# Kernel optimization log

Hardware: AMD Instinct MI355X
Metric: run time of the kernel (lower is better)

Reference implementation:

```python
import jax, jax.numpy as jnp
import numpy as np
import math

L, H, P = 16384, 128, 256


def setup_inputs() -> dict:
    key = jax.random.key(0)
    k = jax.random.split(key, 6)
    return {
        "input_sequence": jax.random.normal(k[0], (L, H), dtype=jnp.float32),
        "A_diag": jax.random.uniform(k[1], (P,), dtype=jnp.float32),
        "B": (jax.random.uniform(k[2], (P, H, 2), dtype=jnp.float32) * 2.0 - 1.0) / math.sqrt(H),
        "C": (jax.random.uniform(k[3], (H, P, 2), dtype=jnp.float32) * 2.0 - 1.0) / math.sqrt(P),
        "D": jax.random.normal(k[4], (H,), dtype=jnp.float32),
        "steps": jax.random.uniform(k[5], (P,), dtype=jnp.float32),
    }


def _binop(qi, qj):
    # 2x2 block-diagonal matrix product + affine state propagation, per channel.
    iA, iB, iC, iD, ib1, ib2 = qi
    jA, jB, jC, jD, jb1, jb2 = qj
    return (
        jA * iA + jB * iC,
        jA * iB + jB * iD,
        jC * iA + jD * iC,
        jC * iB + jD * iD,
        jA * ib1 + jB * ib2 + jb1,
        jC * ib1 + jD * ib2 + jb2,
    )


def reference(input_sequence, A_diag, B, C, D, steps):
    # LinOSS-IM discretization (implicit)
    A = jax.nn.relu(A_diag)                      # (P,)
    dt = jax.nn.sigmoid(steps)                   # (P,)
    Bc = B[..., 0] + 1j * B[..., 1]              # (P,H) complex64
    Cc = C[..., 0] + 1j * C[..., 1]              # (H,P) complex64

    Bu = input_sequence @ Bc.T                   # (L,P) complex64

    schur = 1.0 / (1.0 + dt ** 2 * A)
    M11 = 1.0 - dt ** 2 * A * schur
    M12 = -dt * A * schur
    M21 = dt * schur
    M22 = schur

    ones = jnp.ones((input_sequence.shape[0], A.shape[0]), dtype=input_sequence.dtype)
    F1 = M11 * Bu * dt                           # (L,P) complex
    F2 = M21 * Bu * dt

    elems = (M11 * ones, M12 * ones, M21 * ones, M22 * ones, F1, F2)
    _, _, _, _, _, x2 = jax.lax.associative_scan(_binop, elems)  # scan over L

    ys = jnp.real(x2 @ Cc.T)                     # (L,H)
    return ys + input_sequence * D
```

## Files before the change

kernel.cpp:

```cpp
#include <hip/hip_runtime.h>
#include <math.h>

#define L 16384
#define H 128
#define P 256
#define CL 32
#define NCH (L/CL)
#define GS 16
#define NG (NCH/GS)
#define KDIM 512
#define NBU 512

typedef __attribute__((ext_vector_type(8))) short short8;
typedef __attribute__((ext_vector_type(4))) float f32x4;

__device__ inline unsigned short f2bf(float f){
  union { float f; unsigned u; } v; v.f = f;
  unsigned u = v.u;
  u += 0x7fffu + ((u >> 16) & 1u);
  return (unsigned short)(u >> 16);
}
__device__ inline float bf2f(unsigned short s){
  union { unsigned u; float f; } v; v.u = ((unsigned)s) << 16;
  return v.f;
}

struct Params { float M11,M12,M21,M22,s1,s2; };

__device__ inline Params get_params(const float* A_diag, const float* steps, int p){
  float A = A_diag[p]; A = A > 0.f ? A : 0.f;
  float dt = 1.f/(1.f + expf(-steps[p]));
  float schur = 1.f/(1.f + dt*dt*A);
  Params q;
  q.M11 = 1.f - dt*dt*A*schur;
  q.M12 = -dt*A*schur;
  q.M21 = dt*schur;
  q.M22 = schur;
  q.s1 = q.M11*dt;
  q.s2 = q.M21*dt;
  return q;
}

__device__ inline unsigned long long aload(const unsigned long long* p){
  return __hip_atomic_load((unsigned long long*)p, __ATOMIC_RELAXED,
                           __HIP_MEMORY_SCOPE_AGENT);
}
__device__ inline void apub(unsigned long long* p, unsigned long long v){
  (void)__hip_atomic_exchange(p, v, __ATOMIC_RELAXED, __HIP_MEMORY_SCOPE_AGENT);
}
__device__ inline void fpub(unsigned* p){
  (void)__hip_atomic_exchange(p, 1u, __ATOMIC_RELAXED, __HIP_MEMORY_SCOPE_AGENT);
}
__device__ inline void wait_flag(unsigned* f){
  while (__hip_atomic_load(f, __ATOMIC_RELAXED, __HIP_MEMORY_SCOPE_AGENT) == 0u)
    __builtin_amdgcn_s_sleep(1);
}

__device__ inline void chunk_bu_to_lds(int c, const float* __restrict__ in,
                                       const unsigned short* __restrict__ BWswz,
                                       unsigned short (*sBu)[NBU+8]){
  int tid = threadIdx.x;
  int lane = tid & 63, w = tid >> 6;
  int ml = lane & 15, quad = lane >> 4;
  int mt = w & 1, ng = w >> 1;
  int lm0 = mt*16;
  const float* aptr = in + (size_t)(c*CL + lm0 + ml)*H + quad*8;
  short8 av[4];
  #pragma unroll
  for (int ks=0; ks<4; ks++){
    float4 f0 = *(const float4*)(aptr + ks*32);
    float4 f1 = *(const float4*)(aptr + ks*32 + 4);
    union { short8 s; unsigned short u[8]; } o;
    o.u[0]=f2bf(f0.x); o.u[1]=f2bf(f0.y); o.u[2]=f2bf(f0.z); o.u[3]=f2bf(f0.w);
    o.u[4]=f2bf(f1.x); o.u[5]=f2bf(f1.y); o.u[6]=f2bf(f1.z); o.u[7]=f2bf(f1.w);
    av[ks] = o.s;
  }
  f32x4 acc[8];
  #pragma unroll
  for (int t=0;t<8;t++) acc[t] = (f32x4){0.f,0.f,0.f,0.f};
  #pragma unroll
  for (int ks=0; ks<4; ks++){
    #pragma unroll
    for (int t=0;t<8;t++){
      int n0 = (ng*8 + t)*16;
      short8 bv = *(const short8*)(BWswz + ((size_t)(ks*4+quad)*NBU + n0 + ml)*8);
      acc[t] = __builtin_amdgcn_mfma_f32_16x16x32_bf16(av[ks], bv, acc[t], 0, 0, 0);
    }
  }
  #pragma unroll
  for (int t=0;t<8;t++){
    int n = (ng*8+t)*16 + ml;
    #pragma unroll
    for (int r=0;r<4;r++)
      sBu[lm0 + quad*4 + r][n] = f2bf(acc[t][r]);
  }
}

__global__ __launch_bounds__(512) void prep_w(const float* __restrict__ B,
                                              const float* __restrict__ Cw,
                                              unsigned short* __restrict__ BWswz,
                                              unsigned short* __restrict__ Bswz,
                                              unsigned* __restrict__ flags){
  int gidx = blockIdx.x*512 + threadIdx.x;
  if (gidx < NCH + NG + 1) flags[gidx] = 0u;
  if (gidx < H*NBU){
    int k = gidx >> 9, n = gidx & 511;
    int p = n & 255, c2 = n >> 8;
    float v = B[((size_t)p*H + k)*2 + c2];
    BWswz[((size_t)(k>>3)*NBU + n)*8 + (k&7)] = f2bf(v);
  } else {
    int g2 = gidx - H*NBU;
    int k = g2 >> 7, n = g2 & 127;
    float v = (k < P) ? Cw[((size_t)n*P + k)*2]
                      : -Cw[((size_t)n*P + (k-P))*2 + 1];
    Bswz[((size_t)(k>>3)*H + n)*8 + (k&7)] = f2bf(v);
  }
}

__global__ __launch_bounds__(512, 4) void linoss_fused(
    const float* __restrict__ in,
    const float* __restrict__ A_diag,
    const float* __restrict__ steps,
    const float* __restrict__ Dv,
    const unsigned short* __restrict__ BWswz,
    const unsigned short* __restrict__ Bswz,
    unsigned long long* __restrict__ finals,
    unsigned long long* __restrict__ gfin,
    unsigned* __restrict__ flag1,
    unsigned* __restrict__ flag2,
    unsigned* __restrict__ counter,
    float* __restrict__ out)
{
  __shared__ unsigned short sX[CL][NBU+8];
  __shared__ int s_cid;
  const int tid = threadIdx.x;
  if (tid == 0)
    s_cid = (int)__hip_atomic_fetch_add(counter, 1u, __ATOMIC_RELAXED,
                                        __HIP_MEMORY_SCOPE_AGENT);
  __syncthreads();
  const int c = s_cid;

  chunk_bu_to_lds(c, in, BWswz, sX);
  __syncthreads();

  const int p = tid & 255, part = tid >> 8;
  Params q = get_params(A_diag, steps, p);
  float Ta=q.M11, Tb=q.M12, Tc=q.M21, Td=q.M22;
  #pragma unroll
  for (int s=0;s<5;s++){
    float na=Ta*Ta+Tb*Tc, nb=Ta*Tb+Tb*Td, nc=Tc*Ta+Td*Tc, nd=Tc*Tb+Td*Td;
    Ta=na;Tb=nb;Tc=nc;Td=nd;
  }
  float fx1=0.f, fx2=0.f;
  {
    float u[CL];
    #pragma unroll
    for (int i=0;i<CL;i++) u[i] = bf2f(sX[i][part*256 + p]);
    #pragma unroll
    for (int i=0;i<CL;i++){
      float n1 = q.M11*fx1 + q.M12*fx2 + q.s1*u[i];
      float n2 = q.M21*fx1 + q.M22*fx2 + q.s2*u[i];
      fx1 = n1; fx2 = n2;
    }
  }
  {
    union { unsigned long long u; float2 f; } w; w.f = make_float2(fx1,fx2);
    apub(&finals[(size_t)(part*NCH + c)*P + p], w.u);
  }
  asm volatile("s_waitcnt vmcnt(0)" ::: "memory");
  __syncthreads();
  if (tid == 0) fpub(&flag1[c]);

  const int g = c >> 4, iw = c & (GS-1);
  const unsigned long long* Fp = finals + (size_t)part*NCH*P + (size_t)g*GS*P + p;

  float z1=0.f, z2v=0.f;
  bool have_z = false;
  if (iw == GS-1){
    if (tid < GS-1) wait_flag(&flag1[g*GS + tid]);
    __syncthreads();
    unsigned long long v[GS-1];
    #pragma unroll
    for (int j=0;j<GS-1;j++) v[j] = aload(Fp + (size_t)j*P);
    #pragma unroll
    for (int j=0;j<GS-1;j++){
      union { unsigned long long u; float2 f; } w; w.u = v[j];
      float n1 = Ta*z1 + Tb*z2v + w.f.x;
      float n2 = Tc*z1 + Td*z2v + w.f.y;
      z1=n1; z2v=n2;
    }
    have_z = true;
    float t1 = Ta*z1 + Tb*z2v + fx1;
    float t2 = Tc*z1 + Td*z2v + fx2;
    union { unsigned long long u; float2 f; } w; w.f = make_float2(t1,t2);
    apub(&gfin[(size_t)(part*NG + g)*P + p], w.u);
    asm volatile("s_waitcnt vmcnt(0)" ::: "memory");
    __syncthreads();
    if (tid == 0) fpub(&flag2[g]);
  }

  float sa=1.f, sb=0.f, sc=0.f, sd=1.f;
  {
    float wa=Ta, wb=Tb, wc=Tc, wd=Td;
    #pragma unroll
    for (int bit=0; bit<4; bit++){
      if ((iw>>bit)&1){
        float na = wa*sa + wb*sc, nb = wa*sb + wb*sd;
        float nc = wc*sa + wd*sc, nd = wc*sb + wd*sd;
        sa=na; sb=nb; sc=nc; sd=nd;
      }
      float qa = wa*wa + wb*wc, qb = wa*wb + wb*wd;
      float qc = wc*wa + wd*wc, qd = wc*wb + wd*wd;
      wa=qa; wb=qb; wc=qc; wd=qd;
    }
  }
  float ga=Ta, gb=Tb, gc=Tc, gd=Td;
  #pragma unroll
  for (int s=0;s<4;s++){
    float na=ga*ga+gb*gc, nb=ga*gb+gb*gd, nc=gc*ga+gd*gc, nd=gc*gb+gd*gd;
    ga=na;gb=nb;gc=nc;gd=nd;
  }

  if (tid < g)                             wait_flag(&flag2[tid]);
  if (!have_z && tid >= 64 && tid < 64+iw) wait_flag(&flag1[g*GS + (tid-64)]);
  __syncthreads();

  {
    float y1=0.f, y2=0.f;
    {
      const unsigned long long* Gp = gfin + (size_t)part*NG*P + p;
      #pragma unroll
      for (int half=0; half<2; half++){
        unsigned long long v[16];
        #pragma unroll
        for (int j=0;j<16;j++) v[j] = aload(Gp + (size_t)(half*16+j)*P);
        #pragma unroll
        for (int j=0;j<16;j++){
          int jj = half*16+j;
          if (jj < g){
            union { unsigned long long u; float2 f; } w; w.u = v[j];
            float n1 = ga*y1 + gb*y2 + w.f.x;
            float n2 = gc*y1 + gd*y2 + w.f.y;
            y1=n1; y2=n2;
          }
        }
      }
    }
    if (!have_z){
      unsigned long long v[GS-1];
      #pragma unroll
      for (int j=0;j<GS-1;j++) v[j] = aload(Fp + (size_t)j*P);
      #pragma unroll
      for (int j=0;j<GS-1;j++){
        if (j < iw){
          union { unsigned long long u; float2 f; } w; w.u = v[j];
          float n1 = Ta*z1 + Tb*z2v + w.f.x;
          float n2 = Tc*z1 + Td*z2v + w.f.y;
          z1=n1; z2v=n2;
        }
      }
    }
    float x1 = sa*y1 + sb*y2 + z1;
    float x2 = sc*y1 + sd*y2 + z2v;
    float u[CL];
    #pragma unroll
    for (int i=0;i<CL;i++) u[i] = bf2f(sX[i][part*256 + p]);
    unsigned short hw[CL];
    #pragma unroll
    for (int i=0;i<CL;i++){
      float n1 = q.M11*x1 + q.M12*x2 + q.s1*u[i];
      float n2 = q.M21*x1 + q.M22*x2 + q.s2*u[i];
      x1 = n1; x2 = n2;
      hw[i] = f2bf(x2);
    }
    #pragma unroll
    for (int i=0;i<CL;i++) sX[i][part*256 + p] = hw[i];
  }
  __syncthreads();

  {
    int lane = tid & 63, w = tid >> 6;
    int ml = lane & 15, quad = lane >> 4;
    int mt = w & 1;
    int ntb = (w >> 1) * 2;
    f32x4 acc[2];
    acc[0] = (f32x4){0.f,0.f,0.f,0.f};
    acc[1] = (f32x4){0.f,0.f,0.f,0.f};
    for (int ks=0; ks<KDIM/32; ks++){
      short8 av = *(const short8*)&sX[mt*16 + ml][ks*32 + quad*8];
      #pragma unroll
      for (int j=0;j<2;j++){
        short8 bv = *(const short8*)(Bswz + ((size_t)(ks*4+quad)*H + (ntb+j)*16 + ml)*8);
        acc[j] = __builtin_amdgcn_mfma_f32_16x16x32_bf16(av, bv, acc[j], 0, 0, 0);
      }
    }
    #pragma unroll
    for (int j=0;j<2;j++){
      int h = (ntb+j)*16 + ml;
      float dv = Dv[h];
      #pragma unroll
      for (int r=0;r<4;r++){
        int l = c*CL + mt*16 + quad*4 + r;
        out[(size_t)l*H + h] = acc[j][r] + in[(size_t)l*H + h]*dv;
      }
    }
  }
}

extern "C" void kernel_launch(void* const* d_in, const int* in_sizes, int n_in,
                              void* d_out, int out_size, void* d_ws, size_t ws_size,
                              hipStream_t stream) {
  const float* in     = (const float*)d_in[0];
  const float* A_diag = (const float*)d_in[1];
  const float* B      = (const float*)d_in[2];
  const float* Cw     = (const float*)d_in[3];
  const float* Dv     = (const float*)d_in[4];
  const float* steps  = (const float*)d_in[5];
  float* out = (float*)d_out;

  unsigned short* BWswz = (unsigned short*)d_ws;
  unsigned short* Bswz  = BWswz + (size_t)H*NBU;
  unsigned long long* finals = (unsigned long long*)(Bswz + (size_t)KDIM*H);
  unsigned long long* gfin   = finals + (size_t)2*NCH*P;
  unsigned* flags = (unsigned*)(gfin + (size_t)2*NG*P);
  unsigned* flag1 = flags;
  unsigned* flag2 = flags + NCH;
  unsigned* counter = flags + NCH + NG;

  prep_w<<<256, 512, 0, stream>>>(B, Cw, BWswz, Bswz, flags);
  linoss_fused<<<NCH, 512, 0, stream>>>(in, A_diag, steps, Dv, BWswz, Bswz,
                                        finals, gfin, flag1, flag2, counter, out);
}
```

Before: 105.2 us.

## Replace serial group-prefix chain with Kogge-Stone style cross-block scan levels

```diff
diff --git a/kernel.cpp b/kernel.cpp
--- a/kernel.cpp
+++ b/kernel.cpp
@@ -8,6 +8,7 @@
 #define NCH (L/CL)
 #define GS 16
 #define NG (NCH/GS)
+#define NLEV 5
 #define KDIM 512
 #define NBU 512
 
@@ -102,7 +103,7 @@
                                               unsigned short* __restrict__ Bswz,
                                               unsigned* __restrict__ flags){
   int gidx = blockIdx.x*512 + threadIdx.x;
-  if (gidx < NCH + NG + 1) flags[gidx] = 0u;
+  if (gidx < NCH + (NLEV+1)*NG + 1) flags[gidx] = 0u;
   if (gidx < H*NBU){
     int k = gidx >> 9, n = gidx & 511;
     int p = n & 255, c2 = n >> 8;
@@ -125,9 +126,9 @@
     const unsigned short* __restrict__ BWswz,
     const unsigned short* __restrict__ Bswz,
     unsigned long long* __restrict__ finals,
-    unsigned long long* __restrict__ gfin,
+    unsigned long long* __restrict__ ylev,
     unsigned* __restrict__ flag1,
-    unsigned* __restrict__ flag2,
+    unsigned* __restrict__ kflag,
     unsigned* __restrict__ counter,
     float* __restrict__ out)
 {
@@ -174,31 +175,6 @@
   const int g = c >> 4, iw = c & (GS-1);
   const unsigned long long* Fp = finals + (size_t)part*NCH*P + (size_t)g*GS*P + p;
 
-  float z1=0.f, z2v=0.f;
-  bool have_z = false;
-  if (iw == GS-1){
-    if (tid < GS-1) wait_flag(&flag1[g*GS + tid]);
-    __syncthreads();
-    unsigned long long v[GS-1];
-    #pragma unroll
-    for (int j=0;j<GS-1;j++) v[j] = aload(Fp + (size_t)j*P);
-    #pragma unroll
-    for (int j=0;j<GS-1;j++){
-      union { unsigned long long u; float2 f; } w; w.u = v[j];
-      float n1 = Ta*z1 + Tb*z2v + w.f.x;
-      float n2 = Tc*z1 + Td*z2v + w.f.y;
-      z1=n1; z2v=n2;
-    }
-    have_z = true;
-    float t1 = Ta*z1 + Tb*z2v + fx1;
-    float t2 = Tc*z1 + Td*z2v + fx2;
-    union { unsigned long long u; float2 f; } w; w.f = make_float2(t1,t2);
-    apub(&gfin[(size_t)(part*NG + g)*P + p], w.u);
-    asm volatile("s_waitcnt vmcnt(0)" ::: "memory");
-    __syncthreads();
-    if (tid == 0) fpub(&flag2[g]);
-  }
-
   float sa=1.f, sb=0.f, sc=0.f, sd=1.f;
   {
     float wa=Ta, wb=Tb, wc=Tc, wd=Td;
@@ -221,45 +197,69 @@
     ga=na;gb=nb;gc=nc;gd=nd;
   }
 
-  if (tid < g)                             wait_flag(&flag2[tid]);
-  if (!have_z && tid >= 64 && tid < 64+iw) wait_flag(&flag1[g*GS + (tid-64)]);
-  __syncthreads();
-
-  {
-    float y1=0.f, y2=0.f;
+  float z1=0.f, z2v=0.f;
+  {
+    if (tid < iw) wait_flag(&flag1[g*GS + tid]);
+    __syncthreads();
+    unsigned long long v[GS-1];
+    #pragma unroll
+    for (int j=0;j<GS-1;j++)
+      if (j < iw) v[j] = aload(Fp + (size_t)j*P);
+    #pragma unroll
+    for (int j=0;j<GS-1;j++){
+      if (j < iw){
+        union { unsigned long long u; float2 f; } w; w.u = v[j];
+        float n1 = Ta*z1 + Tb*z2v + w.f.x;
+        float n2 = Tc*z1 + Td*z2v + w.f.y;
+        z1=n1; z2v=n2;
+      }
+    }
+  }
+
+  if (iw == GS-1){
+    float v1 = Ta*z1 + Tb*z2v + fx1;
+    float v2 = Tc*z1 + Td*z2v + fx2;
     {
-      const unsigned long long* Gp = gfin + (size_t)part*NG*P + p;
-      #pragma unroll
-      for (int half=0; half<2; half++){
-        unsigned long long v[16];
-        #pragma unroll
-        for (int j=0;j<16;j++) v[j] = aload(Gp + (size_t)(half*16+j)*P);
-        #pragma unroll
-        for (int j=0;j<16;j++){
-          int jj = half*16+j;
-          if (jj < g){
-            union { unsigned long long u; float2 f; } w; w.u = v[j];
-            float n1 = ga*y1 + gb*y2 + w.f.x;
-            float n2 = gc*y1 + gd*y2 + w.f.y;
-            y1=n1; y2=n2;
-          }
-        }
-      }
-    }
-    if (!have_z){
-      unsigned long long v[GS-1];
-      #pragma unroll
-      for (int j=0;j<GS-1;j++) v[j] = aload(Fp + (size_t)j*P);
-      #pragma unroll
-      for (int j=0;j<GS-1;j++){
-        if (j < iw){
-          union { unsigned long long u; float2 f; } w; w.u = v[j];
-          float n1 = Ta*z1 + Tb*z2v + w.f.x;
-          float n2 = Tc*z1 + Td*z2v + w.f.y;
-          z1=n1; z2v=n2;
-        }
-      }
-    }
+      union { unsigned long long u; float2 f; } w; w.f = make_float2(v1,v2);
+      apub(ylev + ((size_t)(0*2+part)*NG + g)*P + p, w.u);
+    }
+    asm volatile("s_waitcnt vmcnt(0)" ::: "memory");
+    __syncthreads();
+    if (tid == 0) fpub(&kflag[0*NG + g]);
+    float pa=ga, pb=gb, pc=gc, pd=gd;
+    #pragma unroll
+    for (int k=0;k<NLEV;k++){
+      if (g >= (1<<k)){
+        if (tid == 0) wait_flag(&kflag[k*NG + (g-(1<<k))]);
+        __syncthreads();
+        union { unsigned long long u; float2 f; } w;
+        w.u = aload(ylev + ((size_t)(k*2+part)*NG + (g-(1<<k)))*P + p);
+        float n1 = pa*w.f.x + pb*w.f.y + v1;
+        float n2 = pc*w.f.x + pd*w.f.y + v2;
+        v1=n1; v2=n2;
+      }
+      { float na=pa*pa+pb*pc, nb=pa*pb+pb*pd, nc=pc*pa+pd*pc, nd=pc*pb+pd*pd;
+        pa=na;pb=nb;pc=nc;pd=nd; }
+      {
+        union { unsigned long long u; float2 f; } w; w.f = make_float2(v1,v2);
+        apub(ylev + ((size_t)((k+1)*2+part)*NG + g)*P + p, w.u);
+      }
+      asm volatile("s_waitcnt vmcnt(0)" ::: "memory");
+      __syncthreads();
+      if (tid == 0) fpub(&kflag[(k+1)*NG + g]);
+    }
+  }
+
+  float y1=0.f, y2=0.f;
+  if (g > 0){
+    if (tid == 0) wait_flag(&kflag[NLEV*NG + (g-1)]);
+    __syncthreads();
+    union { unsigned long long u; float2 f; } w;
+    w.u = aload(ylev + ((size_t)(NLEV*2+part)*NG + (g-1))*P + p);
+    y1 = w.f.x; y2 = w.f.y;
+  }
+
+  {
     float x1 = sa*y1 + sb*y2 + z1;
     float x2 = sc*y1 + sd*y2 + z2v;
     float u[CL];
@@ -321,13 +321,13 @@
   unsigned short* BWswz = (unsigned short*)d_ws;
   unsigned short* Bswz  = BWswz + (size_t)H*NBU;
   unsigned long long* finals = (unsigned long long*)(Bswz + (size_t)KDIM*H);
-  unsigned long long* gfin   = finals + (size_t)2*NCH*P;
-  unsigned* flags = (unsigned*)(gfin + (size_t)2*NG*P);
+  unsigned long long* ylev   = finals + (size_t)2*NCH*P;
+  unsigned* flags = (unsigned*)(ylev + (size_t)(NLEV+1)*2*NG*P);
   unsigned* flag1 = flags;
-  unsigned* flag2 = flags + NCH;
-  unsigned* counter = flags + NCH + NG;
+  unsigned* kflag = flags + NCH;
+  unsigned* counter = flags + NCH + (NLEV+1)*NG;
 
   prep_w<<<256, 512, 0, stream>>>(B, Cw, BWswz, Bswz, flags);
   linoss_fused<<<NCH, 512, 0, stream>>>(in, A_diag, steps, Dv, BWswz, Bswz,
-                                        finals, gfin, flag1, flag2, counter, out);
-}
+                                        finals, ylev, flag1, kflag, counter, out);
+}
```

New measurement: 108.7 us. +3.3%, slower.

## Use per-wave completion flags and unify intra-group prefix computation in fused scan

Applied to the files above, without the earlier changes.

```diff
diff --git a/kernel.cpp b/kernel.cpp
--- a/kernel.cpp
+++ b/kernel.cpp
@@ -8,8 +8,10 @@
 #define NCH (L/CL)
 #define GS 16
 #define NG (NCH/GS)
+#define FW 8
 #define KDIM 512
 #define NBU 512
+#define NFLAGS (NCH*FW + NG*FW + 1)
 
 typedef __attribute__((ext_vector_type(8))) short short8;
 typedef __attribute__((ext_vector_type(4))) float f32x4;
@@ -56,53 +58,13 @@
     __builtin_amdgcn_s_sleep(1);
 }
 
-__device__ inline void chunk_bu_to_lds(int c, const float* __restrict__ in,
-                                       const unsigned short* __restrict__ BWswz,
-                                       unsigned short (*sBu)[NBU+8]){
-  int tid = threadIdx.x;
-  int lane = tid & 63, w = tid >> 6;
-  int ml = lane & 15, quad = lane >> 4;
-  int mt = w & 1, ng = w >> 1;
-  int lm0 = mt*16;
-  const float* aptr = in + (size_t)(c*CL + lm0 + ml)*H + quad*8;
-  short8 av[4];
-  #pragma unroll
-  for (int ks=0; ks<4; ks++){
-    float4 f0 = *(const float4*)(aptr + ks*32);
-    float4 f1 = *(const float4*)(aptr + ks*32 + 4);
-    union { short8 s; unsigned short u[8]; } o;
-    o.u[0]=f2bf(f0.x); o.u[1]=f2bf(f0.y); o.u[2]=f2bf(f0.z); o.u[3]=f2bf(f0.w);
-    o.u[4]=f2bf(f1.x); o.u[5]=f2bf(f1.y); o.u[6]=f2bf(f1.z); o.u[7]=f2bf(f1.w);
-    av[ks] = o.s;
-  }
-  f32x4 acc[8];
-  #pragma unroll
-  for (int t=0;t<8;t++) acc[t] = (f32x4){0.f,0.f,0.f,0.f};
-  #pragma unroll
-  for (int ks=0; ks<4; ks++){
-    #pragma unroll
-    for (int t=0;t<8;t++){
-      int n0 = (ng*8 + t)*16;
-      short8 bv = *(const short8*)(BWswz + ((size_t)(ks*4+quad)*NBU + n0 + ml)*8);
-      acc[t] = __builtin_amdgcn_mfma_f32_16x16x32_bf16(av[ks], bv, acc[t], 0, 0, 0);
-    }
-  }
-  #pragma unroll
-  for (int t=0;t<8;t++){
-    int n = (ng*8+t)*16 + ml;
-    #pragma unroll
-    for (int r=0;r<4;r++)
-      sBu[lm0 + quad*4 + r][n] = f2bf(acc[t][r]);
-  }
-}
-
 __global__ __launch_bounds__(512) void prep_w(const float* __restrict__ B,
                                               const float* __restrict__ Cw,
                                               unsigned short* __restrict__ BWswz,
                                               unsigned short* __restrict__ Bswz,
                                               unsigned* __restrict__ flags){
   int gidx = blockIdx.x*512 + threadIdx.x;
-  if (gidx < NCH + NG + 1) flags[gidx] = 0u;
+  if (gidx < NFLAGS) flags[gidx] = 0u;
   if (gidx < H*NBU){
     int k = gidx >> 9, n = gidx & 511;
     int p = n & 255, c2 = n >> 8;
@@ -117,7 +79,7 @@
   }
 }
 
-__global__ __launch_bounds__(512, 4) void linoss_fused(
+__global__ __launch_bounds__(512, 2) void linoss_fused(
     const float* __restrict__ in,
     const float* __restrict__ A_diag,
     const float* __restrict__ steps,
@@ -140,7 +102,49 @@
   __syncthreads();
   const int c = s_cid;
 
-  chunk_bu_to_lds(c, in, BWswz, sX);
+  {
+    int lane = tid & 63, w = tid >> 6;
+    int ml = lane & 15, quad = lane >> 4;
+    int mt = w & 1, ng = w >> 1;
+    int lm0 = mt*16;
+    const float* aptr = in + (size_t)(c*CL + lm0 + ml)*H + quad*8;
+    float4 fa[8];
+    #pragma unroll
+    for (int ks=0; ks<4; ks++){
+      fa[2*ks]   = *(const float4*)(aptr + ks*32);
+      fa[2*ks+1] = *(const float4*)(aptr + ks*32 + 4);
+    }
+    short8 av[4];
+    #pragma unroll
+    for (int ks=0; ks<4; ks++){
+      union { short8 s; unsigned short u[8]; } o;
+      o.u[0]=f2bf(fa[2*ks].x); o.u[1]=f2bf(fa[2*ks].y);
+      o.u[2]=f2bf(fa[2*ks].z); o.u[3]=f2bf(fa[2*ks].w);
+      o.u[4]=f2bf(fa[2*ks+1].x); o.u[5]=f2bf(fa[2*ks+1].y);
+      o.u[6]=f2bf(fa[2*ks+1].z); o.u[7]=f2bf(fa[2*ks+1].w);
+      av[ks] = o.s;
+    }
+    f32x4 acc[8];
+    #pragma unroll
+    for (int t=0;t<8;t++) acc[t] = (f32x4){0.f,0.f,0.f,0.f};
+    #pragma unroll
+    for (int ks=0; ks<4; ks++){
+      short8 bv[8];
+      #pragma unroll
+      for (int t=0;t<8;t++)
+        bv[t] = *(const short8*)(BWswz + ((size_t)(ks*4+quad)*NBU + (ng*8+t)*16 + ml)*8);
+      #pragma unroll
+      for (int t=0;t<8;t++)
+        acc[t] = __builtin_amdgcn_mfma_f32_16x16x32_bf16(av[ks], bv[t], acc[t], 0, 0, 0);
+    }
+    #pragma unroll
+    for (int t=0;t<8;t++){
+      int n = (ng*8+t)*16 + ml;
+      #pragma unroll
+      for (int r=0;r<4;r++)
+        sX[lm0 + quad*4 + r][n] = f2bf(acc[t][r]);
+    }
+  }
   __syncthreads();
 
   const int p = tid & 255, part = tid >> 8;
@@ -168,36 +172,10 @@
     apub(&finals[(size_t)(part*NCH + c)*P + p], w.u);
   }
   asm volatile("s_waitcnt vmcnt(0)" ::: "memory");
-  __syncthreads();
-  if (tid == 0) fpub(&flag1[c]);
+  if ((tid & 63) == 0) fpub(&flag1[c*FW + (tid >> 6)]);
 
   const int g = c >> 4, iw = c & (GS-1);
   const unsigned long long* Fp = finals + (size_t)part*NCH*P + (size_t)g*GS*P + p;
-
-  float z1=0.f, z2v=0.f;
-  bool have_z = false;
-  if (iw == GS-1){
-    if (tid < GS-1) wait_flag(&flag1[g*GS + tid]);
-    __syncthreads();
-    unsigned long long v[GS-1];
-    #pragma unroll
-    for (int j=0;j<GS-1;j++) v[j] = aload(Fp + (size_t)j*P);
-    #pragma unroll
-    for (int j=0;j<GS-1;j++){
-      union { unsigned long long u; float2 f; } w; w.u = v[j];
-      float n1 = Ta*z1 + Tb*z2v + w.f.x;
-      float n2 = Tc*z1 + Td*z2v + w.f.y;
-      z1=n1; z2v=n2;
-    }
-    have_z = true;
-    float t1 = Ta*z1 + Tb*z2v + fx1;
-    float t2 = Tc*z1 + Td*z2v + fx2;
-    union { unsigned long long u; float2 f; } w; w.f = make_float2(t1,t2);
-    apub(&gfin[(size_t)(part*NG + g)*P + p], w.u);
-    asm volatile("s_waitcnt vmcnt(0)" ::: "memory");
-    __syncthreads();
-    if (tid == 0) fpub(&flag2[g]);
-  }
 
   float sa=1.f, sb=0.f, sc=0.f, sd=1.f;
   {
@@ -221,8 +199,35 @@
     ga=na;gb=nb;gc=nc;gd=nd;
   }
 
-  if (tid < g)                             wait_flag(&flag2[tid]);
-  if (!have_z && tid >= 64 && tid < 64+iw) wait_flag(&flag1[g*GS + (tid-64)]);
+  float z1=0.f, z2v=0.f;
+  {
+    if (tid < iw*FW) wait_flag(&flag1[(g*GS + (tid>>3))*FW + (tid&7)]);
+    __syncthreads();
+    unsigned long long v[GS-1];
+    #pragma unroll
+    for (int j=0;j<GS-1;j++)
+      if (j < iw) v[j] = aload(Fp + (size_t)j*P);
+    #pragma unroll
+    for (int j=0;j<GS-1;j++){
+      if (j < iw){
+        union { unsigned long long u; float2 f; } w; w.u = v[j];
+        float n1 = Ta*z1 + Tb*z2v + w.f.x;
+        float n2 = Tc*z1 + Td*z2v + w.f.y;
+        z1=n1; z2v=n2;
+      }
+    }
+  }
+
+  if (iw == GS-1){
+    float t1 = Ta*z1 + Tb*z2v + fx1;
+    float t2 = Tc*z1 + Td*z2v + fx2;
+    union { unsigned long long u; float2 f; } w; w.f = make_float2(t1,t2);
+    apub(&gfin[(size_t)(part*NG + g)*P + p], w.u);
+    asm volatile("s_waitcnt vmcnt(0)" ::: "memory");
+    if ((tid & 63) == 0) fpub(&flag2[g*FW + (tid >> 6)]);
+  }
+
+  if (tid < g*FW) wait_flag(&flag2[tid]);
   __syncthreads();
 
   {
@@ -233,7 +238,10 @@
       for (int half=0; half<2; half++){
         unsigned long long v[16];
         #pragma unroll
-        for (int j=0;j<16;j++) v[j] = aload(Gp + (size_t)(half*16+j)*P);
+        for (int j=0;j<16;j++){
+          int jj = half*16+j;
+          if (jj < g) v[j] = aload(Gp + (size_t)jj*P);
+        }
         #pragma unroll
         for (int j=0;j<16;j++){
           int jj = half*16+j;
@@ -246,20 +254,6 @@
         }
       }
     }
-    if (!have_z){
-      unsigned long long v[GS-1];
-      #pragma unroll
-      for (int j=0;j<GS-1;j++) v[j] = aload(Fp + (size_t)j*P);
-      #pragma unroll
-      for (int j=0;j<GS-1;j++){
-        if (j < iw){
-          union { unsigned long long u; float2 f; } w; w.u = v[j];
-          float n1 = Ta*z1 + Tb*z2v + w.f.x;
-          float n2 = Tc*z1 + Td*z2v + w.f.y;
-          z1=n1; z2v=n2;
-        }
-      }
-    }
     float x1 = sa*y1 + sb*y2 + z1;
     float x2 = sc*y1 + sd*y2 + z2v;
     float u[CL];
@@ -288,11 +282,10 @@
     acc[1] = (f32x4){0.f,0.f,0.f,0.f};
     for (int ks=0; ks<KDIM/32; ks++){
       short8 av = *(const short8*)&sX[mt*16 + ml][ks*32 + quad*8];
-      #pragma unroll
-      for (int j=0;j<2;j++){
-        short8 bv = *(const short8*)(Bswz + ((size_t)(ks*4+quad)*H + (ntb+j)*16 + ml)*8);
-        acc[j] = __builtin_amdgcn_mfma_f32_16x16x32_bf16(av, bv, acc[j], 0, 0, 0);
-      }
+      short8 bv0 = *(const short8*)(Bswz + ((size_t)(ks*4+quad)*H + (ntb+0)*16 + ml)*8);
+      short8 bv1 = *(const short8*)(Bswz + ((size_t)(ks*4+quad)*H + (ntb+1)*16 + ml)*8);
+      acc[0] = __builtin_amdgcn_mfma_f32_16x16x32_bf16(av, bv0, acc[0], 0, 0, 0);
+      acc[1] = __builtin_amdgcn_mfma_f32_16x16x32_bf16(av, bv1, acc[1], 0, 0, 0);
     }
     #pragma unroll
     for (int j=0;j<2;j++){
@@ -324,8 +317,8 @@
   unsigned long long* gfin   = finals + (size_t)2*NCH*P;
   unsigned* flags = (unsigned*)(gfin + (size_t)2*NG*P);
   unsigned* flag1 = flags;
-  unsigned* flag2 = flags + NCH;
-  unsigned* counter = flags + NCH + NG;
+  unsigned* flag2 = flags + NCH*FW;
+  unsigned* counter = flags + NCH*FW + NG*FW;
 
   prep_w<<<256, 512, 0, stream>>>(B, Cw, BWswz, Bswz, flags);
   linoss_fused<<<NCH, 512, 0, stream>>>(in, A_diag, steps, Dv, BWswz, Bswz,
```

Measured after the change: 104.6 us. Within noise of the previous version (-0.6%).
